# Kernel optimization log

Measured on AMD Instinct MI355X. Metric: run time of the kernel, lower is better.

## Reference

```python
import jax, jax.numpy as jnp
import numpy as np

D_MODEL = 1024
HIDDEN = 4096
N_EXPERTS = 8
TOP_K = 2


def setup_inputs() -> dict:
    key = jax.random.key(0)
    k_x, k_r, k_w1, k_w2 = jax.random.split(key, 4)
    x = jax.random.normal(k_x, (2, 1024, D_MODEL), dtype=jnp.float32)
    # router: nn.Linear(d_model, n_experts, bias=False) -> weight [E, D]; store transposed [D, E]
    Wr = jax.random.normal(k_r, (D_MODEL, N_EXPERTS), dtype=jnp.float32) * 0.02
    # expert w1: Linear(D, H) -> store [E, D, H]; w2: Linear(H, D) -> [E, H, D]
    W1 = jax.random.normal(k_w1, (N_EXPERTS, D_MODEL, HIDDEN), dtype=jnp.float32) * 0.02
    W2 = jax.random.normal(k_w2, (N_EXPERTS, HIDDEN, D_MODEL), dtype=jnp.float32) * 0.02
    return {"x": x, "Wr": Wr, "W1": W1, "W2": W2}


def reference(x, Wr, W1, W2):
    B, S, D = x.shape
    flat = x.reshape(-1, D)                       # [T, D]
    logits = flat @ Wr                            # [T, E]
    top_vals, top_idx = jax.lax.top_k(logits, TOP_K)
    # softmax over the top-k logits; forward only uses slot 0 (faithful to source)
    weights = jax.nn.softmax(top_vals, axis=-1)   # [T, K]
    top1 = top_idx[:, 0]                          # [T] int
    w_top1 = weights[:, 0]                        # [T]
    # dense all-expert compute (fixed small E loop fused into batched einsum)
    h = jax.nn.gelu(jnp.einsum('td,edh->teh', flat, W1), approximate=False)  # [T,E,H]
    y = jnp.einsum('teh,ehd->ted', h, W2)         # [T, E, D]
    y_sel = jnp.take_along_axis(y, top1[:, None, None], axis=1)[:, 0, :]     # [T, D]
    out = (w_top1[:, None] * y_sel).reshape(B, S, D)
    return out
```

## Files before the change

### kernel.cpp

```cpp
#include <hip/hip_runtime.h>
#include <hip/hip_bf16.h>
#include <math.h>

#define T_TOKENS 2048
#define DMODEL   1024
#define HID      4096
#define NEXP     8
#define MAX_TILES 32

typedef float  f32x4  __attribute__((ext_vector_type(4)));
typedef short  bf16x8 __attribute__((ext_vector_type(8)));
typedef unsigned short u16x8 __attribute__((ext_vector_type(8)));

__device__ __forceinline__ unsigned short f2bf(float f) {
    union { float f; unsigned u; } v; v.f = f;
    unsigned u = v.u;
    unsigned r = (u + 0x7FFFu + ((u >> 16) & 1u)) >> 16;
    return (unsigned short)r;
}

__device__ __forceinline__ void async_copy16(const void* g, void* l) {
    __builtin_amdgcn_global_load_lds(
        (const __attribute__((address_space(1))) void*)g,
        (__attribute__((address_space(3))) void*)l,
        16, 0, 0);
}

__global__ void router_kernel(const float* __restrict__ x, const float* __restrict__ Wr,
                              int* counts, int* expert_of, int* slot_of, float* wt_of) {
    int t = blockIdx.x;
    int lane = threadIdx.x;
    const float* xr = x + (size_t)t * DMODEL;
    float p[NEXP];
#pragma unroll
    for (int e = 0; e < NEXP; ++e) p[e] = 0.f;
    for (int d = lane; d < DMODEL; d += 64) {
        float xv = xr[d];
        const float* wr = Wr + (size_t)d * NEXP;
#pragma unroll
        for (int e = 0; e < NEXP; ++e) p[e] += xv * wr[e];
    }
#pragma unroll
    for (int e = 0; e < NEXP; ++e) {
        for (int off = 32; off > 0; off >>= 1)
            p[e] += __shfl_down(p[e], off, 64);
    }
    if (lane == 0) {
        int i0 = 0; float v0 = p[0];
        for (int e = 1; e < NEXP; ++e) if (p[e] > v0) { v0 = p[e]; i0 = e; }
        float v1 = -INFINITY;
        for (int e = 0; e < NEXP; ++e) if (e != i0 && p[e] > v1) v1 = p[e];
        float w = 1.f / (1.f + expf(v1 - v0));
        expert_of[t] = i0;
        wt_of[t] = w;
        slot_of[t] = atomicAdd(&counts[i0], 1);
    }
}

__global__ void scan_kernel(const int* counts, int* offsets,
                            int* tileE, int* tileM, int* tileCount) {
    if (threadIdx.x == 0 && blockIdx.x == 0) {
        int run = 0, tc = 0;
        for (int e = 0; e < NEXP; ++e) {
            offsets[e] = run;
            for (int m0 = 0; m0 < counts[e]; m0 += 128) {
                tileE[tc] = e; tileM[tc] = m0; ++tc;
            }
            run += counts[e];
        }
        *tileCount = tc;
    }
}

__global__ void scatter_kernel(const int* offsets, const int* expert_of,
                               const int* slot_of, int* perm) {
    int t = blockIdx.x * blockDim.x + threadIdx.x;
    if (t < T_TOKENS) perm[offsets[expert_of[t]] + slot_of[t]] = t;
}

__global__ __launch_bounds__(256) void convert_transpose_kernel(
    const float* __restrict__ W, unsigned short* __restrict__ WT, int K, int N) {
    int ktiles = K >> 6, ntiles = N >> 6;
    int gid = blockIdx.x;
    int e   = gid / (ktiles * ntiles);
    int r   = gid % (ktiles * ntiles);
    int kt  = r / ntiles, nt = r % ntiles;
    const float* src = W + (size_t)e * K * N + (size_t)(kt * 64) * N + nt * 64;
    unsigned short* dst = WT + (size_t)e * N * K + (size_t)(nt * 64) * K + kt * 64;

    __shared__ unsigned short tile[64][66];
    int tid = threadIdx.x;
    int n4 = (tid & 15) * 4;
    int kk = tid >> 4;
#pragma unroll
    for (int p = 0; p < 4; ++p) {
        int k = kk + p * 16;
        float4 v = *(const float4*)(src + (size_t)k * N + n4);
        tile[n4 + 0][k] = f2bf(v.x);
        tile[n4 + 1][k] = f2bf(v.y);
        tile[n4 + 2][k] = f2bf(v.z);
        tile[n4 + 3][k] = f2bf(v.w);
    }
    __syncthreads();
    int n = tid >> 2, ks = (tid & 3) * 16;
    unsigned short tmp[16];
#pragma unroll
    for (int i = 0; i < 16; ++i) tmp[i] = tile[n][ks + i];
    *(u16x8*)(dst + (size_t)n * K + ks)     = *(u16x8*)&tmp[0];
    *(u16x8*)(dst + (size_t)n * K + ks + 8) = *(u16x8*)&tmp[8];
}

__global__ __launch_bounds__(256) void convert_x_kernel(
    const float* __restrict__ x, unsigned short* __restrict__ xbf) {
    int i = (blockIdx.x * 256 + threadIdx.x) * 4;
    float4 v = *(const float4*)(x + i);
    ushort4 b;
    b.x = f2bf(v.x); b.y = f2bf(v.y); b.z = f2bf(v.z); b.w = f2bf(v.w);
    *(ushort4*)(xbf + i) = b;
}

__global__ __launch_bounds__(256, 2) void gemm1_kernel(
    const unsigned short* __restrict__ Xbf, const unsigned short* __restrict__ W1T,
    const int* __restrict__ counts, const int* __restrict__ offsets,
    const int* __restrict__ perm, const int* __restrict__ tileE,
    const int* __restrict__ tileM, const int* __restrict__ tileCount,
    unsigned short* __restrict__ H) {

    const int NT = HID / 128;
    int tile = blockIdx.x / NT;
    int nt   = blockIdx.x % NT;
    if (tile >= *tileCount) return;
    int e = tileE[tile], m0 = tileM[tile];
    int rows_e = counts[e], base = offsets[e];
    int n0 = nt * 128;

    __shared__ unsigned short Alds[128 * 64];
    __shared__ unsigned short Blds[128 * 64];

    int tid  = threadIdx.x;
    int lane = tid & 63;
    int wid  = tid >> 6;
    int wm = wid >> 1, wn = wid & 1;

    const unsigned short* ag[4]; const unsigned short* bg[4];
    unsigned short* al[4]; unsigned short* bl[4];
#pragma unroll
    for (int p = 0; p < 4; ++p) {
        int idx = p * 256 + tid;
        int row = idx >> 3, seg = idx & 7;
        int r = m0 + row;
        int tok = perm[base + (r < rows_e ? r : rows_e - 1)];
        ag[p] = Xbf + (size_t)tok * DMODEL + seg * 8;
        bg[p] = W1T + ((size_t)e * HID + n0 + row) * DMODEL + seg * 8;
        al[p] = &Alds[idx * 8];
        bl[p] = &Blds[idx * 8];
    }

    f32x4 acc[4][4];
#pragma unroll
    for (int i = 0; i < 4; ++i)
#pragma unroll
        for (int j = 0; j < 4; ++j) acc[i][j] = (f32x4){0.f, 0.f, 0.f, 0.f};

    for (int k0 = 0; k0 < DMODEL; k0 += 64) {
        __syncthreads();
#pragma unroll
        for (int p = 0; p < 4; ++p) {
            async_copy16(ag[p] + k0, al[p]);
            async_copy16(bg[p] + k0, bl[p]);
        }
        __syncthreads();
#pragma unroll
        for (int ks = 0; ks < 2; ++ks) {
            int kq = ks * 32 + (lane >> 4) * 8;
            bf16x8 af[4], bfr[4];
#pragma unroll
            for (int i = 0; i < 4; ++i) {
                int m = wm * 64 + i * 16 + (lane & 15);
                af[i] = *(const bf16x8*)&Alds[m * 64 + kq];
                int n = wn * 64 + i * 16 + (lane & 15);
                bfr[i] = *(const bf16x8*)&Blds[n * 64 + kq];
            }
#pragma unroll
            for (int i = 0; i < 4; ++i)
#pragma unroll
                for (int j = 0; j < 4; ++j)
                    acc[i][j] = __builtin_amdgcn_mfma_f32_16x16x32_bf16(af[i], bfr[j], acc[i][j], 0, 0, 0);
        }
    }

    int quad = lane >> 4, col = lane & 15;
#pragma unroll
    for (int i = 0; i < 4; ++i)
#pragma unroll
        for (int j = 0; j < 4; ++j)
#pragma unroll
            for (int r = 0; r < 4; ++r) {
                int ml = wm * 64 + i * 16 + quad * 4 + r;
                if (m0 + ml < rows_e) {
                    int n = n0 + wn * 64 + j * 16 + col;
                    float v = acc[i][j][r];
                    float g = 0.5f * v * (1.0f + erff(v * 0.70710678118654752f));
                    H[(size_t)(base + m0 + ml) * HID + n] = f2bf(g);
                }
            }
}

__global__ __launch_bounds__(256, 2) void gemm2_kernel(
    const unsigned short* __restrict__ H, const unsigned short* __restrict__ W2T,
    const int* __restrict__ counts, const int* __restrict__ offsets,
    const int* __restrict__ perm, const float* __restrict__ wt_of,
    const int* __restrict__ tileE, const int* __restrict__ tileM,
    const int* __restrict__ tileCount, float* __restrict__ out) {

    const int NT = DMODEL / 128;
    const int SK = 4;
    int tile = blockIdx.x / (NT * SK);
    int rem  = blockIdx.x % (NT * SK);
    int nt   = rem / SK;
    int sk   = rem % SK;
    if (tile >= *tileCount) return;
    int e = tileE[tile], m0 = tileM[tile];
    int rows_e = counts[e], base = offsets[e];
    int n0 = nt * 128;
    int kbeg = sk * (HID / SK), kend = kbeg + (HID / SK);

    __shared__ unsigned short Alds[128 * 64];
    __shared__ unsigned short Blds[128 * 64];
    __shared__ int   rowTok[128];
    __shared__ float rowW[128];

    int tid  = threadIdx.x;
    int lane = tid & 63;
    int wid  = tid >> 6;
    int wm = wid >> 1, wn = wid & 1;

    if (tid < 128) {
        int r = m0 + tid;
        if (r < rows_e) {
            int tok = perm[base + r];
            rowTok[tid] = tok;
            rowW[tid]   = wt_of[tok];
        } else { rowTok[tid] = 0; rowW[tid] = 0.f; }
    }

    const unsigned short* ag[4]; const unsigned short* bg[4];
    unsigned short* al[4]; unsigned short* bl[4];
#pragma unroll
    for (int p = 0; p < 4; ++p) {
        int idx = p * 256 + tid;
        int row = idx >> 3, seg = idx & 7;
        int hr = base + m0 + row;
        if (hr > T_TOKENS - 1) hr = T_TOKENS - 1;
        ag[p] = H + (size_t)hr * HID + seg * 8;
        bg[p] = W2T + ((size_t)e * DMODEL + n0 + row) * HID + seg * 8;
        al[p] = &Alds[idx * 8];
        bl[p] = &Blds[idx * 8];
    }

    f32x4 acc[4][4];
#pragma unroll
    for (int i = 0; i < 4; ++i)
#pragma unroll
        for (int j = 0; j < 4; ++j) acc[i][j] = (f32x4){0.f, 0.f, 0.f, 0.f};

    for (int k0 = kbeg; k0 < kend; k0 += 64) {
        __syncthreads();
#pragma unroll
        for (int p = 0; p < 4; ++p) {
            async_copy16(ag[p] + k0, al[p]);
            async_copy16(bg[p] + k0, bl[p]);
        }
        __syncthreads();
#pragma unroll
        for (int ks = 0; ks < 2; ++ks) {
            int kq = ks * 32 + (lane >> 4) * 8;
            bf16x8 af[4], bfr[4];
#pragma unroll
            for (int i = 0; i < 4; ++i) {
                int m = wm * 64 + i * 16 + (lane & 15);
                af[i] = *(const bf16x8*)&Alds[m * 64 + kq];
                int n = wn * 64 + i * 16 + (lane & 15);
                bfr[i] = *(const bf16x8*)&Blds[n * 64 + kq];
            }
#pragma unroll
            for (int i = 0; i < 4; ++i)
#pragma unroll
                for (int j = 0; j < 4; ++j)
                    acc[i][j] = __builtin_amdgcn_mfma_f32_16x16x32_bf16(af[i], bfr[j], acc[i][j], 0, 0, 0);
        }
    }

    int quad = lane >> 4, col = lane & 15;
#pragma unroll
    for (int i = 0; i < 4; ++i)
#pragma unroll
        for (int j = 0; j < 4; ++j)
#pragma unroll
            for (int r = 0; r < 4; ++r) {
                int ml = wm * 64 + i * 16 + quad * 4 + r;
                if (m0 + ml < rows_e) {
                    int tok = rowTok[ml];
                    float w = rowW[ml];
                    int n = n0 + wn * 64 + j * 16 + col;
                    atomicAdd(&out[(size_t)tok * DMODEL + n], w * acc[i][j][r]);
                }
            }
}

extern "C" void kernel_launch(void* const* d_in, const int* in_sizes, int n_in,
                              void* d_out, int out_size, void* d_ws, size_t ws_size,
                              hipStream_t stream) {
    const float* x  = (const float*)d_in[0];
    const float* Wr = (const float*)d_in[1];
    const float* W1 = (const float*)d_in[2];
    const float* W2 = (const float*)d_in[3];
    float* out = (float*)d_out;

    char* ws = (char*)d_ws;
    int*   counts    = (int*)(ws);
    int*   offsets   = (int*)(ws + 64);
    int*   tileCount = (int*)(ws + 128);
    int*   tileE     = (int*)(ws + 256);
    int*   tileM     = (int*)(ws + 256 + 4 * MAX_TILES);
    int*   expert_of = (int*)(ws + 1024);
    int*   slot_of   = (int*)(ws + 1024 + 8192);
    float* wt_of     = (float*)(ws + 1024 + 16384);
    int*   perm      = (int*)(ws + 1024 + 24576);
    size_t off = 65536;
    unsigned short* Xbf = (unsigned short*)(ws + off);               off += (size_t)T_TOKENS * DMODEL * 2;
    unsigned short* Hbuf = (unsigned short*)(ws + off);              off += (size_t)T_TOKENS * HID * 2;
    unsigned short* W1T = (unsigned short*)(ws + off);               off += (size_t)NEXP * DMODEL * HID * 2;
    unsigned short* W2T = (unsigned short*)(ws + off);

    hipMemsetAsync(counts, 0, 64, stream);
    hipMemsetAsync(out, 0, (size_t)T_TOKENS * DMODEL * sizeof(float), stream);

    router_kernel<<<T_TOKENS, 64, 0, stream>>>(x, Wr, counts, expert_of, slot_of, wt_of);
    scan_kernel<<<1, 64, 0, stream>>>(counts, offsets, tileE, tileM, tileCount);
    scatter_kernel<<<T_TOKENS / 256, 256, 0, stream>>>(offsets, expert_of, slot_of, perm);

    convert_x_kernel<<<(T_TOKENS * DMODEL) / 1024, 256, 0, stream>>>(x, Xbf);
    convert_transpose_kernel<<<NEXP * (DMODEL / 64) * (HID / 64), 256, 0, stream>>>(W1, W1T, DMODEL, HID);
    convert_transpose_kernel<<<NEXP * (HID / 64) * (DMODEL / 64), 256, 0, stream>>>(W2, W2T, HID, DMODEL);

    gemm1_kernel<<<MAX_TILES * (HID / 128), 256, 0, stream>>>(
        Xbf, W1T, counts, offsets, perm, tileE, tileM, tileCount, Hbuf);
    gemm2_kernel<<<MAX_TILES * (DMODEL / 128) * 4, 256, 0, stream>>>(
        Hbuf, W2T, counts, offsets, perm, wt_of, tileE, tileM, tileCount, out);
}
```

Baseline: 444.7 us.

## Fuse weight bf16 conversion into GEMM loads with double-buffered swizzled LDS

Drops the separate weight convert-transpose kernels. The GEMMs now read fp32 W1/W2 directly, convert them to bf16 in registers with a packed convert, and write a transposed, XOR-swizzled tile into double-buffered LDS. The aim is to avoid the full weight round trip through memory (read fp32, write bf16, read again) and overlap the loads with the MFMA work. The x conversion is folded into the router, and scan and scatter are merged into one kernel, which removes launches. In exchange, each GEMM tile converts its weights again and issues non-async fp32 loads, which adds register pressure and raw bandwidth per tile.

New measurement: 438.2 us. Within noise of the previous version (-1.4%).

```diff
diff --git a/kernel.cpp b/kernel.cpp
--- a/kernel.cpp
+++ b/kernel.cpp
@@ -1,5 +1,4 @@
 #include <hip/hip_runtime.h>
-#include <hip/hip_bf16.h>
 #include <math.h>
 
 #define T_TOKENS 2048
@@ -10,7 +9,6 @@
 
 typedef float  f32x4  __attribute__((ext_vector_type(4)));
 typedef short  bf16x8 __attribute__((ext_vector_type(8)));
-typedef unsigned short u16x8 __attribute__((ext_vector_type(8)));
 
 __device__ __forceinline__ unsigned short f2bf(float f) {
     union { float f; unsigned u; } v; v.f = f;
@@ -19,6 +17,16 @@
     return (unsigned short)r;
 }
 
+__device__ __forceinline__ unsigned pk2bf(float lo, float hi) {
+    unsigned r;
+    asm("v_cvt_pk_bf16_f32 %0, %1, %2" : "=v"(r) : "v"(lo), "v"(hi));
+    return r;
+}
+
+__device__ __forceinline__ float f4get(const float4& v, int i) {
+    return i == 0 ? v.x : i == 1 ? v.y : i == 2 ? v.z : v.w;
+}
+
 __device__ __forceinline__ void async_copy16(const void* g, void* l) {
     __builtin_amdgcn_global_load_lds(
         (const __attribute__((address_space(1))) void*)g,
@@ -26,19 +34,31 @@
         16, 0, 0);
 }
 
-__global__ void router_kernel(const float* __restrict__ x, const float* __restrict__ Wr,
-                              int* counts, int* expert_of, int* slot_of, float* wt_of) {
+__global__ __launch_bounds__(64) void router_kernel(
+    const float* __restrict__ x, const float* __restrict__ Wr,
+    int* counts, int* expert_of, int* slot_of, float* wt_of,
+    unsigned short* __restrict__ Xbf) {
     int t = blockIdx.x;
     int lane = threadIdx.x;
     const float* xr = x + (size_t)t * DMODEL;
+    unsigned short* xb = Xbf + (size_t)t * DMODEL;
     float p[NEXP];
 #pragma unroll
     for (int e = 0; e < NEXP; ++e) p[e] = 0.f;
-    for (int d = lane; d < DMODEL; d += 64) {
-        float xv = xr[d];
-        const float* wr = Wr + (size_t)d * NEXP;
-#pragma unroll
-        for (int e = 0; e < NEXP; ++e) p[e] += xv * wr[e];
+#pragma unroll
+    for (int q = 0; q < 4; ++q) {
+        int d = q * 256 + lane * 4;
+        float4 v = *(const float4*)(xr + d);
+        ushort4 b;
+        b.x = f2bf(v.x); b.y = f2bf(v.y); b.z = f2bf(v.z); b.w = f2bf(v.w);
+        *(ushort4*)(xb + d) = b;
+#pragma unroll
+        for (int j = 0; j < 4; ++j) {
+            float xv = f4get(v, j);
+            const float* wr = Wr + (size_t)(d + j) * NEXP;
+#pragma unroll
+            for (int e = 0; e < NEXP; ++e) p[e] += xv * wr[e];
+        }
     }
 #pragma unroll
     for (int e = 0; e < NEXP; ++e) {
@@ -57,12 +77,15 @@
     }
 }
 
-__global__ void scan_kernel(const int* counts, int* offsets,
-                            int* tileE, int* tileM, int* tileCount) {
-    if (threadIdx.x == 0 && blockIdx.x == 0) {
+__global__ void scan_scatter_kernel(const int* counts, int* offsets,
+                                    int* tileE, int* tileM, int* tileCount,
+                                    const int* expert_of, const int* slot_of,
+                                    int* perm) {
+    __shared__ int soff[NEXP];
+    if (threadIdx.x == 0) {
         int run = 0, tc = 0;
         for (int e = 0; e < NEXP; ++e) {
-            offsets[e] = run;
+            offsets[e] = run; soff[e] = run;
             for (int m0 = 0; m0 < counts[e]; m0 += 128) {
                 tileE[tc] = e; tileM[tc] = m0; ++tc;
             }
@@ -70,57 +93,13 @@
         }
         *tileCount = tc;
     }
-}
-
-__global__ void scatter_kernel(const int* offsets, const int* expert_of,
-                               const int* slot_of, int* perm) {
-    int t = blockIdx.x * blockDim.x + threadIdx.x;
-    if (t < T_TOKENS) perm[offsets[expert_of[t]] + slot_of[t]] = t;
-}
-
-__global__ __launch_bounds__(256) void convert_transpose_kernel(
-    const float* __restrict__ W, unsigned short* __restrict__ WT, int K, int N) {
-    int ktiles = K >> 6, ntiles = N >> 6;
-    int gid = blockIdx.x;
-    int e   = gid / (ktiles * ntiles);
-    int r   = gid % (ktiles * ntiles);
-    int kt  = r / ntiles, nt = r % ntiles;
-    const float* src = W + (size_t)e * K * N + (size_t)(kt * 64) * N + nt * 64;
-    unsigned short* dst = WT + (size_t)e * N * K + (size_t)(nt * 64) * K + kt * 64;
-
-    __shared__ unsigned short tile[64][66];
-    int tid = threadIdx.x;
-    int n4 = (tid & 15) * 4;
-    int kk = tid >> 4;
-#pragma unroll
-    for (int p = 0; p < 4; ++p) {
-        int k = kk + p * 16;
-        float4 v = *(const float4*)(src + (size_t)k * N + n4);
-        tile[n4 + 0][k] = f2bf(v.x);
-        tile[n4 + 1][k] = f2bf(v.y);
-        tile[n4 + 2][k] = f2bf(v.z);
-        tile[n4 + 3][k] = f2bf(v.w);
-    }
     __syncthreads();
-    int n = tid >> 2, ks = (tid & 3) * 16;
-    unsigned short tmp[16];
-#pragma unroll
-    for (int i = 0; i < 16; ++i) tmp[i] = tile[n][ks + i];
-    *(u16x8*)(dst + (size_t)n * K + ks)     = *(u16x8*)&tmp[0];
-    *(u16x8*)(dst + (size_t)n * K + ks + 8) = *(u16x8*)&tmp[8];
-}
-
-__global__ __launch_bounds__(256) void convert_x_kernel(
-    const float* __restrict__ x, unsigned short* __restrict__ xbf) {
-    int i = (blockIdx.x * 256 + threadIdx.x) * 4;
-    float4 v = *(const float4*)(x + i);
-    ushort4 b;
-    b.x = f2bf(v.x); b.y = f2bf(v.y); b.z = f2bf(v.z); b.w = f2bf(v.w);
-    *(ushort4*)(xbf + i) = b;
+    for (int t = threadIdx.x; t < T_TOKENS; t += blockDim.x)
+        perm[soff[expert_of[t]] + slot_of[t]] = t;
 }
 
 __global__ __launch_bounds__(256, 2) void gemm1_kernel(
-    const unsigned short* __restrict__ Xbf, const unsigned short* __restrict__ W1T,
+    const unsigned short* __restrict__ Xbf, const float* __restrict__ W1,
     const int* __restrict__ counts, const int* __restrict__ offsets,
     const int* __restrict__ perm, const int* __restrict__ tileE,
     const int* __restrict__ tileM, const int* __restrict__ tileCount,
@@ -134,27 +113,32 @@
     int rows_e = counts[e], base = offsets[e];
     int n0 = nt * 128;
 
-    __shared__ unsigned short Alds[128 * 64];
-    __shared__ unsigned short Blds[128 * 64];
+    __shared__ unsigned short Alds[2][128 * 64];
+    __shared__ unsigned short Blds[2][128 * 64];
 
     int tid  = threadIdx.x;
     int lane = tid & 63;
     int wid  = tid >> 6;
     int wm = wid >> 1, wn = wid & 1;
-
-    const unsigned short* ag[4]; const unsigned short* bg[4];
-    unsigned short* al[4]; unsigned short* bl[4];
+    const int swz = (lane & 7) << 4;
+
+    const unsigned short* ag[4];
+    int aoff[4];
 #pragma unroll
     for (int p = 0; p < 4; ++p) {
         int idx = p * 256 + tid;
-        int row = idx >> 3, seg = idx & 7;
+        int row = idx >> 3;
+        int seg = (idx & 7) ^ (row & 7);
         int r = m0 + row;
         int tok = perm[base + (r < rows_e ? r : rows_e - 1)];
         ag[p] = Xbf + (size_t)tok * DMODEL + seg * 8;
-        bg[p] = W1T + ((size_t)e * HID + n0 + row) * DMODEL + seg * 8;
-        al[p] = &Alds[idx * 8];
-        bl[p] = &Blds[idx * 8];
-    }
+        aoff[p] = idx * 16;
+    }
+
+    const int kq4 = (tid & 15) * 4;
+    const int nb  = (tid >> 4) * 8;
+    const float* bsrc = W1 + ((size_t)e * DMODEL + kq4) * HID + n0 + nb;
+    float4 breg[8];
 
     f32x4 acc[4][4];
 #pragma unroll
@@ -162,31 +146,67 @@
 #pragma unroll
         for (int j = 0; j < 4; ++j) acc[i][j] = (f32x4){0.f, 0.f, 0.f, 0.f};
 
-    for (int k0 = 0; k0 < DMODEL; k0 += 64) {
+#define G_ISSUE(kt, BUF, STRIDE) do {                                         \
+    _Pragma("unroll")                                                         \
+    for (int r_ = 0; r_ < 4; ++r_) {                                          \
+        _Pragma("unroll")                                                     \
+        for (int q_ = 0; q_ < 2; ++q_)                                        \
+            breg[r_*2+q_] = *(const float4*)(bsrc + ((size_t)(kt)*64 + r_) * (STRIDE) + q_*4); \
+    }                                                                         \
+    _Pragma("unroll")                                                         \
+    for (int p_ = 0; p_ < 4; ++p_)                                            \
+        async_copy16(ag[p_] + (kt) * 64, (char*)Alds[BUF] + aoff[p_]);        \
+} while (0)
+
+#define G_WRITEB(BUF) do {                                                    \
+    char* bb_ = (char*)Blds[BUF];                                             \
+    _Pragma("unroll")                                                         \
+    for (int j_ = 0; j_ < 8; ++j_) {                                          \
+        unsigned lo_ = pk2bf(f4get(breg[0 + (j_>>2)], j_&3),                  \
+                             f4get(breg[2 + (j_>>2)], j_&3));                 \
+        unsigned hi_ = pk2bf(f4get(breg[4 + (j_>>2)], j_&3),                  \
+                             f4get(breg[6 + (j_>>2)], j_&3));                 \
+        unsigned long long w_ = ((unsigned long long)hi_ << 32) | lo_;        \
+        *(unsigned long long*)(bb_ + (nb + j_) * 128 + ((kq4 * 2) ^ (j_ << 4))) = w_; \
+    }                                                                         \
+} while (0)
+
+#define G_COMPUTE(BUF) do {                                                   \
+    const char* ab_ = (const char*)Alds[BUF];                                 \
+    const char* bb_ = (const char*)Blds[BUF];                                 \
+    _Pragma("unroll")                                                         \
+    for (int ks_ = 0; ks_ < 2; ++ks_) {                                       \
+        int kb_ = (ks_ * 32 + ((lane >> 4) * 8)) * 2;                         \
+        bf16x8 af_[4], bf_[4];                                                \
+        _Pragma("unroll")                                                     \
+        for (int i_ = 0; i_ < 4; ++i_) {                                      \
+            int m_ = wm * 64 + i_ * 16 + (lane & 15);                         \
+            af_[i_] = *(const bf16x8*)(ab_ + m_ * 128 + (kb_ ^ swz));         \
+            int n_ = wn * 64 + i_ * 16 + (lane & 15);                         \
+            bf_[i_] = *(const bf16x8*)(bb_ + n_ * 128 + (kb_ ^ swz));         \
+        }                                                                     \
+        _Pragma("unroll")                                                     \
+        for (int i_ = 0; i_ < 4; ++i_)                                        \
+            _Pragma("unroll")                                                 \
+            for (int j_ = 0; j_ < 4; ++j_)                                    \
+                acc[i_][j_] = __builtin_amdgcn_mfma_f32_16x16x32_bf16(af_[i_], bf_[j_], acc[i_][j_], 0, 0, 0); \
+    }                                                                         \
+} while (0)
+
+    G_ISSUE(0, 0, HID);
+    G_WRITEB(0);
+    __syncthreads();
+
+#pragma unroll 1
+    for (int t = 0; t < 16; t += 2) {
+        G_ISSUE(t + 1, 1, HID);
+        G_COMPUTE(0);
+        G_WRITEB(1);
         __syncthreads();
-#pragma unroll
-        for (int p = 0; p < 4; ++p) {
-            async_copy16(ag[p] + k0, al[p]);
-            async_copy16(bg[p] + k0, bl[p]);
-        }
+        if (t + 2 < 16) G_ISSUE(t + 2, 0, HID);
+        G_COMPUTE(1);
+        if (t + 2 < 16) G_WRITEB(0);
         __syncthreads();
-#pragma unroll
-        for (int ks = 0; ks < 2; ++ks) {
-            int kq = ks * 32 + (lane >> 4) * 8;
-            bf16x8 af[4], bfr[4];
-#pragma unroll
-            for (int i = 0; i < 4; ++i) {
-                int m = wm * 64 + i * 16 + (lane & 15);
-                af[i] = *(const bf16x8*)&Alds[m * 64 + kq];
-                int n = wn * 64 + i * 16 + (lane & 15);
-                bfr[i] = *(const bf16x8*)&Blds[n * 64 + kq];
-            }
-#pragma unroll
-            for (int i = 0; i < 4; ++i)
-#pragma unroll
-                for (int j = 0; j < 4; ++j)
-                    acc[i][j] = __builtin_amdgcn_mfma_f32_16x16x32_bf16(af[i], bfr[j], acc[i][j], 0, 0, 0);
-        }
     }
 
     int quad = lane >> 4, col = lane & 15;
@@ -207,7 +227,7 @@
 }
 
 __global__ __launch_bounds__(256, 2) void gemm2_kernel(
-    const unsigned short* __restrict__ H, const unsigned short* __restrict__ W2T,
+    const unsigned short* __restrict__ H, const float* __restrict__ W2,
     const int* __restrict__ counts, const int* __restrict__ offsets,
     const int* __restrict__ perm, const float* __restrict__ wt_of,
     const int* __restrict__ tileE, const int* __restrict__ tileM,
@@ -217,16 +237,16 @@
     const int SK = 4;
     int tile = blockIdx.x / (NT * SK);
     int rem  = blockIdx.x % (NT * SK);
-    int nt   = rem / SK;
-    int sk   = rem % SK;
+    int nt   = rem >> 2;
+    int sk   = rem & 3;
     if (tile >= *tileCount) return;
     int e = tileE[tile], m0 = tileM[tile];
     int rows_e = counts[e], base = offsets[e];
     int n0 = nt * 128;
-    int kbeg = sk * (HID / SK), kend = kbeg + (HID / SK);
-
-    __shared__ unsigned short Alds[128 * 64];
-    __shared__ unsigned short Blds[128 * 64];
+    int kbeg = sk * (HID / SK);
+
+    __shared__ unsigned short Alds[2][128 * 64];
+    __shared__ unsigned short Blds[2][128 * 64];
     __shared__ int   rowTok[128];
     __shared__ float rowW[128];
 
@@ -234,6 +254,7 @@
     int lane = tid & 63;
     int wid  = tid >> 6;
     int wm = wid >> 1, wn = wid & 1;
+    const int swz = (lane & 7) << 4;
 
     if (tid < 128) {
         int r = m0 + tid;
@@ -244,19 +265,23 @@
         } else { rowTok[tid] = 0; rowW[tid] = 0.f; }
     }
 
-    const unsigned short* ag[4]; const unsigned short* bg[4];
-    unsigned short* al[4]; unsigned short* bl[4];
+    const unsigned short* ag[4];
+    int aoff[4];
 #pragma unroll
     for (int p = 0; p < 4; ++p) {
         int idx = p * 256 + tid;
-        int row = idx >> 3, seg = idx & 7;
+        int row = idx >> 3;
+        int seg = (idx & 7) ^ (row & 7);
         int hr = base + m0 + row;
         if (hr > T_TOKENS - 1) hr = T_TOKENS - 1;
-        ag[p] = H + (size_t)hr * HID + seg * 8;
-        bg[p] = W2T + ((size_t)e * DMODEL + n0 + row) * HID + seg * 8;
-        al[p] = &Alds[idx * 8];
-        bl[p] = &Blds[idx * 8];
-    }
+        ag[p] = H + (size_t)hr * HID + kbeg + seg * 8;
+        aoff[p] = idx * 16;
+    }
+
+    const int kq4 = (tid & 15) * 4;
+    const int nb  = (tid >> 4) * 8;
+    const float* bsrc = W2 + ((size_t)e * HID + kbeg + kq4) * DMODEL + n0 + nb;
+    float4 breg[8];
 
     f32x4 acc[4][4];
 #pragma unroll
@@ -264,31 +289,20 @@
 #pragma unroll
         for (int j = 0; j < 4; ++j) acc[i][j] = (f32x4){0.f, 0.f, 0.f, 0.f};
 
-    for (int k0 = kbeg; k0 < kend; k0 += 64) {
+    G_ISSUE(0, 0, DMODEL);
+    G_WRITEB(0);
+    __syncthreads();
+
+#pragma unroll 1
+    for (int t = 0; t < 16; t += 2) {
+        G_ISSUE(t + 1, 1, DMODEL);
+        G_COMPUTE(0);
+        G_WRITEB(1);
         __syncthreads();
-#pragma unroll
-        for (int p = 0; p < 4; ++p) {
-            async_copy16(ag[p] + k0, al[p]);
-            async_copy16(bg[p] + k0, bl[p]);
-        }
+        if (t + 2 < 16) G_ISSUE(t + 2, 0, DMODEL);
+        G_COMPUTE(1);
+        if (t + 2 < 16) G_WRITEB(0);
         __syncthreads();
-#pragma unroll
-        for (int ks = 0; ks < 2; ++ks) {
-            int kq = ks * 32 + (lane >> 4) * 8;
-            bf16x8 af[4], bfr[4];
-#pragma unroll
-            for (int i = 0; i < 4; ++i) {
-                int m = wm * 64 + i * 16 + (lane & 15);
-                af[i] = *(const bf16x8*)&Alds[m * 64 + kq];
-                int n = wn * 64 + i * 16 + (lane & 15);
-                bfr[i] = *(const bf16x8*)&Blds[n * 64 + kq];
-            }
-#pragma unroll
-            for (int i = 0; i < 4; ++i)
-#pragma unroll
-                for (int j = 0; j < 4; ++j)
-                    acc[i][j] = __builtin_amdgcn_mfma_f32_16x16x32_bf16(af[i], bfr[j], acc[i][j], 0, 0, 0);
-        }
     }
 
     int quad = lane >> 4, col = lane & 15;
@@ -328,24 +342,18 @@
     float* wt_of     = (float*)(ws + 1024 + 16384);
     int*   perm      = (int*)(ws + 1024 + 24576);
     size_t off = 65536;
-    unsigned short* Xbf = (unsigned short*)(ws + off);               off += (size_t)T_TOKENS * DMODEL * 2;
-    unsigned short* Hbuf = (unsigned short*)(ws + off);              off += (size_t)T_TOKENS * HID * 2;
-    unsigned short* W1T = (unsigned short*)(ws + off);               off += (size_t)NEXP * DMODEL * HID * 2;
-    unsigned short* W2T = (unsigned short*)(ws + off);
+    unsigned short* Xbf  = (unsigned short*)(ws + off); off += (size_t)T_TOKENS * DMODEL * 2;
+    unsigned short* Hbuf = (unsigned short*)(ws + off);
 
     hipMemsetAsync(counts, 0, 64, stream);
     hipMemsetAsync(out, 0, (size_t)T_TOKENS * DMODEL * sizeof(float), stream);
 
-    router_kernel<<<T_TOKENS, 64, 0, stream>>>(x, Wr, counts, expert_of, slot_of, wt_of);
-    scan_kernel<<<1, 64, 0, stream>>>(counts, offsets, tileE, tileM, tileCount);
-    scatter_kernel<<<T_TOKENS / 256, 256, 0, stream>>>(offsets, expert_of, slot_of, perm);
-
-    convert_x_kernel<<<(T_TOKENS * DMODEL) / 1024, 256, 0, stream>>>(x, Xbf);
-    convert_transpose_kernel<<<NEXP * (DMODEL / 64) * (HID / 64), 256, 0, stream>>>(W1, W1T, DMODEL, HID);
-    convert_transpose_kernel<<<NEXP * (HID / 64) * (DMODEL / 64), 256, 0, stream>>>(W2, W2T, HID, DMODEL);
+    router_kernel<<<T_TOKENS, 64, 0, stream>>>(x, Wr, counts, expert_of, slot_of, wt_of, Xbf);
+    scan_scatter_kernel<<<1, 256, 0, stream>>>(counts, offsets, tileE, tileM, tileCount,
+                                               expert_of, slot_of, perm);
 
     gemm1_kernel<<<MAX_TILES * (HID / 128), 256, 0, stream>>>(
-        Xbf, W1T, counts, offsets, perm, tileE, tileM, tileCount, Hbuf);
+        Xbf, W1, counts, offsets, perm, tileE, tileM, tileCount, Hbuf);
     gemm2_kernel<<<MAX_TILES * (DMODEL / 128) * 4, 256, 0, stream>>>(
-        Hbuf, W2T, counts, offsets, perm, wt_of, tileE, tileM, tileCount, out);
-}
+        Hbuf, W2, counts, offsets, perm, wt_of, tileE, tileM, tileCount, out);
+}
```
